# Kernel tuning notes

Measured on AMD Instinct MI355X. Metric: run time of the kernel, lower is better.

## Reference

```python
import jax, jax.numpy as jnp
import numpy as np

B, Ci, H, W_ = 8, 64, 128, 128
C = 2 * Ci  # output channels of the 1x1 conv


def setup_inputs() -> dict:
    key = jax.random.key(0)
    kx, kw, kb = jax.random.split(key, 3)
    x = jax.random.normal(kx, (B, Ci, H, W_), dtype=jnp.float32)
    # Conv2d(Ci, 2*Ci, 1x1) parameters (kaiming-ish scale)
    Wc = jax.random.normal(kw, (C, Ci), dtype=jnp.float32) * (1.0 / np.float32(np.sqrt(Ci)))
    bc = jax.random.normal(kb, (C,), dtype=jnp.float32) * 0.01
    return {"x": x, "Wc": Wc, "bc": bc}


def _local_attention(y):
    # y: [B, C, H, W] conv output. 3x3 neighborhood self-attention, zero padding.
    b, c, h, w = y.shape
    yp = jnp.pad(y, ((0, 0), (0, 0), (1, 1), (1, 1)))
    # patches[:, :, k] = shifted neighborhood k (row-major 3x3, matching F.unfold order)
    patches = jnp.stack(
        [yp[:, :, di:di + h, dj:dj + w] for di in range(3) for dj in range(3)],
        axis=2,
    )  # [B, C, 9, H, W]
    mid = patches[:, :, 4]  # center pixel query, [B, C, H, W]
    scale = np.float32(1.0 / np.sqrt(c))
    scores = jnp.einsum("bcnhw,bchw->bnhw", patches, mid) * scale  # [B, 9, H, W]
    attn = jax.nn.softmax(scores, axis=1)
    out = jnp.einsum("bnhw,bcnhw->bchw", attn, patches)  # [B, C, H, W]
    return out


def reference(x, Wc, bc):
    # 1x1 conv == channel matmul
    y = jnp.einsum("bihw,oi->bohw", x, Wc) + bc[None, :, None, None]
    return _local_attention(y)
```

## Files before the change

kernel.cpp:

```cpp
#include <hip/hip_runtime.h>
#include <hip/hip_fp16.h>

typedef __attribute__((ext_vector_type(8))) _Float16 half8;
typedef __attribute__((ext_vector_type(2))) _Float16 h2v;
typedef __attribute__((ext_vector_type(4))) float floatx4;

#define PXN 204
#define QBASE 26128

__device__ __forceinline__ ushort f2h(float f) {
    union { _Float16 h; ushort u; } cv;
    cv.h = (_Float16)f;
    return cv.u;
}
__device__ __forceinline__ h2v as_h2(unsigned int u) {
    union { unsigned int u; h2v h; } cv;
    cv.u = u;
    return cv.h;
}

__device__ __forceinline__ float gsum8(float v) {
    v += __int_as_float(__builtin_amdgcn_update_dpp(0, __float_as_int(v), 0xB1, 0xF, 0xF, false));
    v += __int_as_float(__builtin_amdgcn_update_dpp(0, __float_as_int(v), 0x4E, 0xF, 0xF, false));
    v += __shfl_xor(v, 4);
    return v;
}

#define LOADROW(S, PROW)                                                            \
    {                                                                               \
        _Pragma("unroll")                                                           \
        for (int dx = 0; dx < 3; ++dx) {                                            \
            int pi = (PROW) * 34 + ox + dx;                                         \
            const char* pp = smc + pi * 128 + ((g * 16) ^ ((pi & 7) << 4));         \
            wlo[S][dx] = *(const uint4*)pp;                                         \
            whi[S][dx] = *(const uint4*)(pp + QBASE);                               \
        }                                                                           \
    }

#define SCORE1(S, DX) ({                                                            \
        uint4 _l = wlo[S][DX], _h = whi[S][DX];                                     \
        float _s0 = 0.f, _s1 = 0.f;                                                 \
        _s0 = __builtin_amdgcn_fdot2(as_h2(_l.x), cfl[0], _s0, false);              \
        _s1 = __builtin_amdgcn_fdot2(as_h2(_l.y), cfl[1], _s1, false);              \
        _s0 = __builtin_amdgcn_fdot2(as_h2(_l.z), cfl[2], _s0, false);              \
        _s1 = __builtin_amdgcn_fdot2(as_h2(_l.w), cfl[3], _s1, false);              \
        _s0 = __builtin_amdgcn_fdot2(as_h2(_h.x), cfh[0], _s0, false);              \
        _s1 = __builtin_amdgcn_fdot2(as_h2(_h.y), cfh[1], _s1, false);              \
        _s0 = __builtin_amdgcn_fdot2(as_h2(_h.z), cfh[2], _s0, false);              \
        _s1 = __builtin_amdgcn_fdot2(as_h2(_h.w), cfh[3], _s1, false);              \
        _s0 + _s1; })

#define PVU(U, A, O0, O1)                                                           \
    { h2v _v = as_h2(U);                                                            \
      O0 = fmaf((float)_v.x, (A), O0); O1 = fmaf((float)_v.y, (A), O1); }
#define PV(S, DX, A)                                                                \
    {                                                                               \
        uint4 _pl = wlo[S][DX], _ph = whi[S][DX];                                   \
        PVU(_pl.x, A, o[0], o[1])  PVU(_pl.y, A, o[2], o[3])                        \
        PVU(_pl.z, A, o[4], o[5])  PVU(_pl.w, A, o[6], o[7])                        \
        PVU(_ph.x, A, o[8], o[9])  PVU(_ph.y, A, o[10], o[11])                      \
        PVU(_ph.z, A, o[12], o[13]) PVU(_ph.w, A, o[14], o[15])                     \
    }

#define ATTN_OY(OY, ST, SM, SB)                                                     \
    {                                                                               \
        h2v cfl[4], cfh[4];                                                         \
        {                                                                           \
            uint4 c0 = wlo[SM][1], c1 = whi[SM][1];                                 \
            cfl[0] = as_h2(c0.x); cfl[1] = as_h2(c0.y);                             \
            cfl[2] = as_h2(c0.z); cfl[3] = as_h2(c0.w);                             \
            cfh[0] = as_h2(c1.x); cfh[1] = as_h2(c1.y);                             \
            cfh[2] = as_h2(c1.z); cfh[3] = as_h2(c1.w);                             \
        }                                                                           \
        float s[9];                                                                 \
        s[0] = SCORE1(ST, 0); s[1] = SCORE1(ST, 1); s[2] = SCORE1(ST, 2);           \
        s[3] = SCORE1(SM, 0); s[4] = SCORE1(SM, 1); s[5] = SCORE1(SM, 2);           \
        s[6] = SCORE1(SB, 0); s[7] = SCORE1(SB, 1); s[8] = SCORE1(SB, 2);           \
        _Pragma("unroll")                                                           \
        for (int n = 0; n < 9; ++n)                                                 \
            s[n] = gsum8(s[n]) * 0.08838834764831845f;             \
        float m = fmaxf(fmaxf(fmaxf(fmaxf(s[0], s[1]), s[2]),           \
                              fmaxf(fmaxf(s[3], s[4]), s[5])),                      \
                        fmaxf(fmaxf(s[6], s[7]), s[8]));                            \
        float e[9], sum = 0.f;                                                      \
        _Pragma("unroll")                                                           \
        for (int n = 0; n < 9; ++n) { e[n] = __expf(s[n] - m); sum += e[n]; }       \
        float o[16];                                                                \
        _Pragma("unroll")                                                           \
        for (int j = 0; j < 16; ++j) o[j] = 0.f;                                    \
        PV(ST, 0, e[0]) PV(ST, 1, e[1]) PV(ST, 2, e[2])                             \
        PV(SM, 0, e[3]) PV(SM, 1, e[4]) PV(SM, 2, e[5])                             \
        PV(SB, 0, e[6]) PV(SB, 1, e[7]) PV(SB, 2, e[8])                             \
        float inv = 1.f / sum;                                                      \
        float* og = out + ((size_t)((b * 128 + g * 16) * 128 + (h0 + (OY)))) * 128  \
                    + w0 + ox;                                                      \
        _Pragma("unroll")                                                           \
        for (int j = 0; j < 16; ++j)                                                \
            og[j * 16384] = o[j] * inv;                                             \
    }

__global__ __launch_bounds__(256, 2)
void attn_conv_fused(const float* __restrict__ x, const float* __restrict__ Wc,
                     const float* __restrict__ bc, float* __restrict__ out) {
    __shared__ __align__(16) unsigned char smem[52240];
    char* smc = (char*)smem;

    const int tid = threadIdx.x;
    const int rid = ((blockIdx.x & 7) << 7) | (blockIdx.x >> 3);
    const int b   = rid >> 7;
    const int h0  = ((rid >> 2) & 31) * 4;
    const int w0  = (rid & 3) * 32;
    const int lane = tid & 63;
    const int wv   = tid >> 6;
    const int col = lane & 15;
    const int kq  = lane >> 4;

    half8 af0[4], af1[4];
    #pragma unroll
    for (int i = 0; i < 4; ++i) {
        int mt = wv + i * 4;
        if (mt < 13) {
            int px  = mt * 16 + col;
            int py  = (px * 965) >> 15;
            int pxx = px - py * 34;
            int gh = min(max(h0 + py - 1, 0), 127);
            int gw = min(max(w0 + pxx - 1, 0), 127);
            const float* xp = x + (size_t)(b * 64) * 16384 + gh * 128 + gw;
            #pragma unroll
            for (int j = 0; j < 8; ++j) {
                af0[i][j] = (_Float16)xp[(kq * 8 + j) << 14];
                af1[i][j] = (_Float16)xp[(32 + kq * 8 + j) << 14];
            }
        }
    }

    half8 bw[8][2];
    float bias[8];
    #pragma unroll
    for (int t = 0; t < 8; ++t) {
        int c = t * 16 + col;
        bias[t] = bc[c];
        #pragma unroll
        for (int half = 0; half < 2; ++half) {
            const float* wp = Wc + c * 64 + half * 32 + kq * 8;
            float4 wa = *(const float4*)wp;
            float4 wb = *(const float4*)(wp + 4);
            half8 f;
            f[0] = (_Float16)wa.x; f[1] = (_Float16)wa.y;
            f[2] = (_Float16)wa.z; f[3] = (_Float16)wa.w;
            f[4] = (_Float16)wb.x; f[5] = (_Float16)wb.y;
            f[6] = (_Float16)wb.z; f[7] = (_Float16)wb.w;
            bw[t][half] = f;
        }
    }

    char* wbase = smc + (col < 8 ? 0 : QBASE);
    const int cb2 = (col & 7) * 2;
    #pragma unroll
    for (int i = 0; i < 4; ++i) {
        int mt = wv + i * 4;
        if (mt < 13) {
            floatx4 acc[8];
            #pragma unroll
            for (int t = 0; t < 8; ++t) acc[t] = (floatx4){0.f, 0.f, 0.f, 0.f};
            #pragma unroll
            for (int t = 0; t < 8; ++t) {
                acc[t] = __builtin_amdgcn_mfma_f32_16x16x32_f16(af0[i], bw[t][0], acc[t], 0, 0, 0);
                acc[t] = __builtin_amdgcn_mfma_f32_16x16x32_f16(af1[i], bw[t][1], acc[t], 0, 0, 0);
            }
            #pragma unroll
            for (int r = 0; r < 4; ++r) {
                int pxr = mt * 16 + kq * 4 + r;
                if (pxr < PXN) {
                    int py  = (pxr * 965) >> 15;
                    int pxx = pxr - py * 34;
                    int gh = h0 + py - 1, gw = w0 + pxx - 1;
                    bool inb = (gh >= 0 && gh < 128 && gw >= 0 && gw < 128);
                    char* prow = wbase + pxr * 128;
                    int swz = (pxr & 7) << 4;
                    #pragma unroll
                    for (int t = 0; t < 8; ++t)
                        *(ushort*)(prow + (((t * 16) ^ swz) + cb2)) =
                            f2h(inb ? (acc[t][r] + bias[t]) : 0.f);
                }
            }
        }
    }
    __syncthreads();

    const int g  = tid & 7;
    const int ox = tid >> 3;
    uint4 wlo[3][3], whi[3][3];

    LOADROW(0, 0) LOADROW(1, 1) LOADROW(2, 2)
    ATTN_OY(0, 0, 1, 2)
    LOADROW(0, 3)
    ATTN_OY(1, 1, 2, 0)
    LOADROW(1, 4)
    ATTN_OY(2, 2, 0, 1)
    LOADROW(2, 5)
    ATTN_OY(3, 0, 1, 2)
}

extern "C" void kernel_launch(void* const* d_in, const int* in_sizes, int n_in,
                              void* d_out, int out_size, void* d_ws, size_t ws_size,
                              hipStream_t stream) {
    const float* x  = (const float*)d_in[0];
    const float* Wc = (const float*)d_in[1];
    const float* bc = (const float*)d_in[2];
    float* out = (float*)d_out;

    dim3 grid(1024);
    dim3 block(256);
    attn_conv_fused<<<grid, block, 0, stream>>>(x, Wc, bc, out);
}
```

Measured before the change: 126.5 us.

## Double block size to 512 threads, splitting channel work across 16 lanes

The block grows from 256 to 512 threads. The conv phase now gives each wave at most 2 of the 13 M-tiles, down from 4. In the attention phase each thread handles 8 channels instead of 16, and the dot-product reduction widens to 16 lanes with an extra shuffle. The goal is more parallelism and fewer registers per thread, so more waves can hide latency. The cost is an extra cross-lane reduction step, and at two blocks per CU each with 52 KB of shared memory, occupancy may be capped by LDS.

```diff
diff --git a/kernel.cpp b/kernel.cpp
--- a/kernel.cpp
+++ b/kernel.cpp
@@ -19,10 +19,11 @@
     return cv.h;
 }
 
-__device__ __forceinline__ float gsum8(float v) {
+__device__ __forceinline__ float gsum16(float v) {
     v += __int_as_float(__builtin_amdgcn_update_dpp(0, __float_as_int(v), 0xB1, 0xF, 0xF, false));
     v += __int_as_float(__builtin_amdgcn_update_dpp(0, __float_as_int(v), 0x4E, 0xF, 0xF, false));
     v += __shfl_xor(v, 4);
+    v += __shfl_xor(v, 8);
     return v;
 }
 
@@ -31,23 +32,17 @@
         _Pragma("unroll")                                                           \
         for (int dx = 0; dx < 3; ++dx) {                                            \
             int pi = (PROW) * 34 + ox + dx;                                         \
-            const char* pp = smc + pi * 128 + ((g * 16) ^ ((pi & 7) << 4));         \
-            wlo[S][dx] = *(const uint4*)pp;                                         \
-            whi[S][dx] = *(const uint4*)(pp + QBASE);                               \
+            w[S][dx] = *(const uint4*)(rbase + pi * 128 + ((gp * 16) ^ ((pi & 7) << 4))); \
         }                                                                           \
     }
 
 #define SCORE1(S, DX) ({                                                            \
-        uint4 _l = wlo[S][DX], _h = whi[S][DX];                                     \
+        uint4 _u = w[S][DX];                                                        \
         float _s0 = 0.f, _s1 = 0.f;                                                 \
-        _s0 = __builtin_amdgcn_fdot2(as_h2(_l.x), cfl[0], _s0, false);              \
-        _s1 = __builtin_amdgcn_fdot2(as_h2(_l.y), cfl[1], _s1, false);              \
-        _s0 = __builtin_amdgcn_fdot2(as_h2(_l.z), cfl[2], _s0, false);              \
-        _s1 = __builtin_amdgcn_fdot2(as_h2(_l.w), cfl[3], _s1, false);              \
-        _s0 = __builtin_amdgcn_fdot2(as_h2(_h.x), cfh[0], _s0, false);              \
-        _s1 = __builtin_amdgcn_fdot2(as_h2(_h.y), cfh[1], _s1, false);              \
-        _s0 = __builtin_amdgcn_fdot2(as_h2(_h.z), cfh[2], _s0, false);              \
-        _s1 = __builtin_amdgcn_fdot2(as_h2(_h.w), cfh[3], _s1, false);              \
+        _s0 = __builtin_amdgcn_fdot2(as_h2(_u.x), cf[0], _s0, false);               \
+        _s1 = __builtin_amdgcn_fdot2(as_h2(_u.y), cf[1], _s1, false);               \
+        _s0 = __builtin_amdgcn_fdot2(as_h2(_u.z), cf[2], _s0, false);               \
+        _s1 = __builtin_amdgcn_fdot2(as_h2(_u.w), cf[3], _s1, false);               \
         _s0 + _s1; })
 
 #define PVU(U, A, O0, O1)                                                           \
@@ -55,22 +50,18 @@
       O0 = fmaf((float)_v.x, (A), O0); O1 = fmaf((float)_v.y, (A), O1); }
 #define PV(S, DX, A)                                                                \
     {                                                                               \
-        uint4 _pl = wlo[S][DX], _ph = whi[S][DX];                                   \
-        PVU(_pl.x, A, o[0], o[1])  PVU(_pl.y, A, o[2], o[3])                        \
-        PVU(_pl.z, A, o[4], o[5])  PVU(_pl.w, A, o[6], o[7])                        \
-        PVU(_ph.x, A, o[8], o[9])  PVU(_ph.y, A, o[10], o[11])                      \
-        PVU(_ph.z, A, o[12], o[13]) PVU(_ph.w, A, o[14], o[15])                     \
+        uint4 _p = w[S][DX];                                                        \
+        PVU(_p.x, A, o[0], o[1])  PVU(_p.y, A, o[2], o[3])                          \
+        PVU(_p.z, A, o[4], o[5])  PVU(_p.w, A, o[6], o[7])                          \
     }
 
 #define ATTN_OY(OY, ST, SM, SB)                                                     \
     {                                                                               \
-        h2v cfl[4], cfh[4];                                                         \
+        h2v cf[4];                                                                  \
         {                                                                           \
-            uint4 c0 = wlo[SM][1], c1 = whi[SM][1];                                 \
-            cfl[0] = as_h2(c0.x); cfl[1] = as_h2(c0.y);                             \
-            cfl[2] = as_h2(c0.z); cfl[3] = as_h2(c0.w);                             \
-            cfh[0] = as_h2(c1.x); cfh[1] = as_h2(c1.y);                             \
-            cfh[2] = as_h2(c1.z); cfh[3] = as_h2(c1.w);                             \
+            uint4 c0 = w[SM][1];                                                    \
+            cf[0] = as_h2(c0.x); cf[1] = as_h2(c0.y);                               \
+            cf[2] = as_h2(c0.z); cf[3] = as_h2(c0.w);                               \
         }                                                                           \
         float s[9];                                                                 \
         s[0] = SCORE1(ST, 0); s[1] = SCORE1(ST, 1); s[2] = SCORE1(ST, 2);           \
@@ -78,28 +69,28 @@
         s[6] = SCORE1(SB, 0); s[7] = SCORE1(SB, 1); s[8] = SCORE1(SB, 2);           \
         _Pragma("unroll")                                                           \
         for (int n = 0; n < 9; ++n)                                                 \
-            s[n] = gsum8(s[n]) * 0.08838834764831845f;             \
+            s[n] = gsum16(s[n]) * 0.08838834764831845f;            \
         float m = fmaxf(fmaxf(fmaxf(fmaxf(s[0], s[1]), s[2]),           \
                               fmaxf(fmaxf(s[3], s[4]), s[5])),                      \
                         fmaxf(fmaxf(s[6], s[7]), s[8]));                            \
         float e[9], sum = 0.f;                                                      \
         _Pragma("unroll")                                                           \
         for (int n = 0; n < 9; ++n) { e[n] = __expf(s[n] - m); sum += e[n]; }       \
-        float o[16];                                                                \
-        _Pragma("unroll")                                                           \
-        for (int j = 0; j < 16; ++j) o[j] = 0.f;                                    \
+        float o[8];                                                                 \
+        _Pragma("unroll")                                                           \
+        for (int j = 0; j < 8; ++j) o[j] = 0.f;                                     \
         PV(ST, 0, e[0]) PV(ST, 1, e[1]) PV(ST, 2, e[2])                             \
         PV(SM, 0, e[3]) PV(SM, 1, e[4]) PV(SM, 2, e[5])                             \
         PV(SB, 0, e[6]) PV(SB, 1, e[7]) PV(SB, 2, e[8])                             \
         float inv = 1.f / sum;                                                      \
-        float* og = out + ((size_t)((b * 128 + g * 16) * 128 + (h0 + (OY)))) * 128  \
-                    + w0 + ox;                                                      \
-        _Pragma("unroll")                                                           \
-        for (int j = 0; j < 16; ++j)                                                \
+        float* og = out + ((size_t)((b * 128 + gp * 16 + hi * 8) * 128              \
+                    + (h0 + (OY)))) * 128 + w0 + ox;                                \
+        _Pragma("unroll")                                                           \
+        for (int j = 0; j < 8; ++j)                                                 \
             og[j * 16384] = o[j] * inv;                                             \
     }
 
-__global__ __launch_bounds__(256, 2)
+__global__ __launch_bounds__(512, 2)
 void attn_conv_fused(const float* __restrict__ x, const float* __restrict__ Wc,
                      const float* __restrict__ bc, float* __restrict__ out) {
     __shared__ __align__(16) unsigned char smem[52240];
@@ -115,10 +106,10 @@
     const int col = lane & 15;
     const int kq  = lane >> 4;
 
-    half8 af0[4], af1[4];
+    half8 af0[2], af1[2];
     #pragma unroll
-    for (int i = 0; i < 4; ++i) {
-        int mt = wv + i * 4;
+    for (int i = 0; i < 2; ++i) {
+        int mt = wv + i * 8;
         if (mt < 13) {
             int px  = mt * 16 + col;
             int py  = (px * 965) >> 15;
@@ -157,8 +148,8 @@
     char* wbase = smc + (col < 8 ? 0 : QBASE);
     const int cb2 = (col & 7) * 2;
     #pragma unroll
-    for (int i = 0; i < 4; ++i) {
-        int mt = wv + i * 4;
+    for (int i = 0; i < 2; ++i) {
+        int mt = wv + i * 8;
         if (mt < 13) {
             floatx4 acc[8];
             #pragma unroll
@@ -188,9 +179,12 @@
     }
     __syncthreads();
 
-    const int g  = tid & 7;
-    const int ox = tid >> 3;
-    uint4 wlo[3][3], whi[3][3];
+    const int g  = tid & 15;
+    const int ox = tid >> 4;
+    const int gp = g & 7;
+    const int hi = g >> 3;
+    const char* rbase = smc + (hi ? QBASE : 0);
+    uint4 w[3][3];
 
     LOADROW(0, 0) LOADROW(1, 1) LOADROW(2, 2)
     ATTN_OY(0, 0, 1, 2)
@@ -211,6 +205,6 @@
     float* out = (float*)d_out;
 
     dim3 grid(1024);
-    dim3 block(256);
+    dim3 block(512);
     attn_conv_fused<<<grid, block, 0, stream>>>(x, Wc, bc, out);
 }
```

Result: slower. 160.5 us (+27.0%).
